# Optimization experiments

Measured on AMD Instinct MI355X. Metric: run time of the kernel, lower is better.

The kernel has to match this reference:

```python
import jax, jax.numpy as jnp
import numpy as np

EPS = 1e-5

def lrelu(x):
    return jnp.where(x >= 0, x, 0.1 * x)

def bn_eval(x, g, b, m, v):
    # eval-mode BatchNorm over the last (channel) axis
    return (x - m) * (g * jax.lax.rsqrt(v + EPS)) + b

def setup_inputs():
    key = jax.random.key(0)
    ks = jax.random.split(key, 12)
    Nq, K, Cin, Fc, Co = 20000, 32, 3, 64, 64
    q_points = jax.random.normal(ks[0], (Nq, Cin), jnp.float32)
    s_points = jax.random.normal(ks[1], (Nq, Cin), jnp.float32)
    feat = jax.random.normal(ks[2], (Nq, Fc), jnp.float32)
    # valid indices 0..Nq (Nq == shadow/pad row appended in forward)
    neighb_inds = jax.random.randint(ks[3], (Nq, K), 0, Nq + 1)
    def w(k, shape, fan_in):
        return jax.random.normal(k, shape, jnp.float32) / np.float32(np.sqrt(fan_in))
    W_pos2 = w(ks[4], (Fc, Cin), Cin)          # convpos2: Conv2d(Cin, Fc, 1)
    W_attn = w(ks[5], (Co * Cin, Fc), Fc)      # convattn: Conv2d(Fc, Co*Cin, 1)
    W_res = w(ks[6], (Co, Fc), Fc)             # residual 1x1 conv
    def bn(k, c):
        k1, k2, k3, k4 = jax.random.split(k, 4)
        return (jax.random.normal(k1, (c,), jnp.float32) * 0.1 + 1.0,
                jax.random.normal(k2, (c,), jnp.float32) * 0.1,
                jax.random.normal(k3, (c,), jnp.float32) * 0.1,
                jax.random.uniform(k4, (c,), jnp.float32) * 0.5 + 0.5)
    bq = bn(ks[7], Fc); bp = bn(ks[8], Cin); b1 = bn(ks[9], Co); br = bn(ks[10], Co)
    return dict(q_points=q_points, s_points=s_points, neighb_inds=neighb_inds, feat=feat,
                W_pos2=W_pos2, W_attn=W_attn, W_res=W_res,
                bnq_g=bq[0], bnq_b=bq[1], bnq_m=bq[2], bnq_v=bq[3],
                bnp_g=bp[0], bnp_b=bp[1], bnp_m=bp[2], bnp_v=bp[3],
                bn1_g=b1[0], bn1_b=b1[1], bn1_m=b1[2], bn1_v=b1[3],
                bnr_g=br[0], bnr_b=br[1], bnr_m=br[2], bnr_v=br[3])

def reference(q_points, s_points, neighb_inds, feat, W_pos2, W_attn, W_res,
              bnq_g, bnq_b, bnq_m, bnq_v, bnp_g, bnp_b, bnp_m, bnp_v,
              bn1_g, bn1_b, bn1_m, bn1_v, bnr_g, bnr_b, bnr_m, bnr_v):
    Nq, Cin = q_points.shape
    Fc = feat.shape[1]
    Co = W_res.shape[0]
    K = neighb_inds.shape[1]
    # append shadow (zero) row for out-of-range neighbor indices
    s_pad = jnp.concatenate([s_points, jnp.zeros((1, Cin), s_points.dtype)], 0)
    f_pad = jnp.concatenate([feat, jnp.zeros((1, Fc), feat.dtype)], 0)
    xg = s_pad[neighb_inds]                      # [Nq,K,Cin] EFR_P gather
    yg = f_pad[neighb_inds]                      # [Nq,K,Fc]  EFR_F gather
    x_v = xg - q_points[:, None, :]              # [Nq,K,Cin] values
    x_q = lrelu(bn_eval(feat, bnq_g, bnq_b, bnq_m, bnq_v))          # [Nq,Fc]
    pos0 = lrelu(bn_eval(s_points, bnp_g, bnp_b, bnp_m, bnp_v))     # [Nq,Cin]
    pos = (pos0[:, None, :] - x_v) @ W_pos2.T                       # [Nq,K,Fc]
    attn = x_q[:, None, :] - yg + pos                               # [Nq,K,Fc]
    attn = jax.nn.softmax(attn / jnp.sqrt(jnp.float32(Fc)), axis=1) # softmax over K
    attn = (attn @ W_attn.T).reshape(Nq, K, Co, Cin)                # [Nq,K,Co,Cin]
    y_e = jnp.einsum('nkoi,nki->nko', attn, x_v)                    # [Nq,K,Co]
    y_e = lrelu(bn_eval(y_e, bn1_g, bn1_b, bn1_m, bn1_v))
    res = bn_eval(yg @ W_res.T, bnr_g, bnr_b, bnr_m, bnr_v)         # [Nq,K,Co]
    y_e = lrelu(y_e + res)
    return y_e.max(axis=1)                                          # [Nq,Co]
```

## Files before the change

### kernel.cpp

```cpp
#include <hip/hip_runtime.h>
#include <math.h>

#define KNB 32
#define FC 64
#define CO 64
#define EPS 1e-5f
#define NBLOCKS 1024
#define CL 0.180336880095853f

typedef __attribute__((ext_vector_type(8))) short short8;
typedef __attribute__((ext_vector_type(4))) float floatx4;

#if __has_builtin(__builtin_amdgcn_exp2f)
#define EXP2F(x) __builtin_amdgcn_exp2f(x)
#else
#define EXP2F(x) exp2f(x)
#endif
#if __has_builtin(__builtin_amdgcn_rcpf)
#define RCPF(x) __builtin_amdgcn_rcpf(x)
#else
#define RCPF(x) (1.f / (x))
#endif

__device__ __forceinline__ unsigned int pkbf(float a, float b) {
    unsigned int ua = (__float_as_uint(a) + 0x8000u) >> 16;
    unsigned int ub = (__float_as_uint(b) + 0x8000u) & 0xFFFF0000u;
    return ua | ub;
}
__device__ __forceinline__ short f2bf(float x) {
    return (short)((__float_as_uint(x) + 0x8000u) >> 16);
}
__device__ __forceinline__ float lrelu(float x) { return fmaxf(x, 0.1f * x); }

__global__ __launch_bounds__(256, 4) void GCT_61272003445298_kernel(
    const float* __restrict__ q_points,
    const float* __restrict__ s_points,
    const int*   __restrict__ neighb,
    const float* __restrict__ feat,
    const float* __restrict__ W_pos2,
    const float* __restrict__ W_attn,
    const float* __restrict__ W_res,
    const float* __restrict__ bnq_g, const float* __restrict__ bnq_b,
    const float* __restrict__ bnq_m, const float* __restrict__ bnq_v,
    const float* __restrict__ bnp_g, const float* __restrict__ bnp_b,
    const float* __restrict__ bnp_m, const float* __restrict__ bnp_v,
    const float* __restrict__ bn1_g, const float* __restrict__ bn1_b,
    const float* __restrict__ bn1_m, const float* __restrict__ bn1_v,
    const float* __restrict__ bnr_g, const float* __restrict__ bnr_b,
    const float* __restrict__ bnr_m, const float* __restrict__ bnr_v,
    float* __restrict__ out, int Nq)
{
    const int t = threadIdx.x;
    const int wv = t >> 6;
    const int lane = t & 63;
    const int cc = lane & 15, quad = lane >> 4;
    const int o = wv * 16 + cc;

    const int qB  = t >> 7;
    const int kg  = lane >> 3;
    const int fqB = (((t >> 6) & 1) << 3) + (lane & 7);

    __shared__ __align__(16) short sA1[64 * 72];
    __shared__ __align__(16) short sA2[64 * 72];
    __shared__ float sXv[64][4];
    __shared__ __align__(16) float sWp2[192];
    __shared__ __align__(16) float sQs[64], sQb[64];

    if (t < 192) sWp2[t] = CL * W_pos2[t];
    if (t < 64) {
        float sc = bnq_g[t] * rsqrtf(bnq_v[t] + EPS);
        sQs[t] = sc; sQb[t] = bnq_b[t] - bnq_m[t] * sc;
    }
    float ps[3], pb[3];
    #pragma unroll
    for (int i = 0; i < 3; ++i) {
        float sc = bnp_g[i] * rsqrtf(bnp_v[i] + EPS);
        ps[i] = sc; pb[i] = bnp_b[i] - bnp_m[i] * sc;
    }
    const float e1s = bn1_g[o] * rsqrtf(bn1_v[o] + EPS);
    const float e1b = bn1_b[o] - bn1_m[o] * e1s;
    const float ers = bnr_g[o] * rsqrtf(bnr_v[o] + EPS);
    const float erb = bnr_b[o] - bnr_m[o] * ers;

    short8 bW[4][2];
    #pragma unroll
    for (int ty = 0; ty < 4; ++ty) {
        const float* wrow = (ty < 3) ? (W_attn + (long)(o * 3 + ty) * FC)
                                     : (W_res  + (long)o * FC);
        #pragma unroll
        for (int ks = 0; ks < 2; ++ks) {
            int k0 = ks * 32 + quad * 8;
            float4 w0 = *(const float4*)(wrow + k0);
            float4 w1 = *(const float4*)(wrow + k0 + 4);
            short8 b;
            b[0] = f2bf(w0.x); b[1] = f2bf(w0.y); b[2] = f2bf(w0.z); b[3] = f2bf(w0.w);
            b[4] = f2bf(w1.x); b[5] = f2bf(w1.y); b[6] = f2bf(w1.z); b[7] = f2bf(w1.w);
            bW[ty][ks] = b;
        }
    }
    __syncthreads();

    float wp[12];
    *(float4*)&wp[0] = *(const float4*)&sWp2[fqB * 12];
    *(float4*)&wp[4] = *(const float4*)&sWp2[fqB * 12 + 4];
    *(float4*)&wp[8] = *(const float4*)&sWp2[fqB * 12 + 8];

    const float4* __restrict__ feat4 = (const float4*)feat;
    const bool xvWriter = ((t & 0x47) == 0);

    const int npair = (Nq + 1) >> 1;
    for (int p = blockIdx.x; p < npair; p += NBLOCKS) {
        const long n0 = 2L * p;
        long n1 = n0 + 1;
        const bool has1 = (n1 < Nq);
        if (!has1) n1 = n0;
        const long nn = qB ? n1 : n0;

        float nqp0 = -q_points[nn * 3 + 0];
        float nqp1 = -q_points[nn * 3 + 1];
        float nqp2 = -q_points[nn * 3 + 2];
        float p0 = lrelu(fmaf(s_points[nn * 3 + 0], ps[0], pb[0]));
        float p1 = lrelu(fmaf(s_points[nn * 3 + 1], ps[1], pb[1]));
        float p2 = lrelu(fmaf(s_points[nn * 3 + 2], ps[2], pb[2]));
        int4 idx4 = *(const int4*)(neighb + nn * KNB + kg * 4);

        float4 qs4 = *(const float4*)&sQs[fqB * 4];
        float4 qb4 = *(const float4*)&sQb[fqB * 4];
        float4 fx  = feat4[(int)(nn * 16) + fqB];
        float4 xqc;
        {
            float x0 = lrelu(fmaf(fx.x, qs4.x, qb4.x));
            float x1 = lrelu(fmaf(fx.y, qs4.y, qb4.y));
            float x2 = lrelu(fmaf(fx.z, qs4.z, qb4.z));
            float x3 = lrelu(fmaf(fx.w, qs4.w, qb4.w));
            xqc.x = fmaf(p0, wp[0], fmaf(p1, wp[1],  fmaf(p2, wp[2],  CL * x0)));
            xqc.y = fmaf(p0, wp[3], fmaf(p1, wp[4],  fmaf(p2, wp[5],  CL * x1)));
            xqc.z = fmaf(p0, wp[6], fmaf(p1, wp[7],  fmaf(p2, wp[8],  CL * x2)));
            xqc.w = fmaf(p0, wp[9], fmaf(p1, wp[10], fmaf(p2, wp[11], CL * x3)));
        }

        float ev[4][4];
        float s0 = 0.f, s1 = 0.f, s2 = 0.f, s3 = 0.f;
        #pragma unroll
        for (int j = 0; j < 4; ++j) {
            const int idx = ((const int*)&idx4)[j];
            const int row = qB * 32 + kg * 4 + j;
            const float sel = (idx < Nq) ? 1.f : 0.f;
            const int idc = (idx < Nq) ? idx : 0;
            float4 y = feat4[idc * 16 + fqB];
            y.x *= sel; y.y *= sel; y.z *= sel; y.w *= sel;
            uint2 pk; pk.x = pkbf(y.x, y.y); pk.y = pkbf(y.z, y.w);
            *(uint2*)(sA2 + row * 72 + fqB * 4) = pk;
            float xv0 = fmaf(s_points[idc * 3 + 0], sel, nqp0);
            float xv1 = fmaf(s_points[idc * 3 + 1], sel, nqp1);
            float xv2 = fmaf(s_points[idc * 3 + 2], sel, nqp2);
            if (xvWriter) {
                sXv[row][0] = xv0; sXv[row][1] = xv1; sXv[row][2] = xv2;
                sXv[row][3] = 0.f;
            }
            float l0 = fmaf(y.x, -CL, xqc.x);
            l0 = fmaf(-xv0, wp[0], l0); l0 = fmaf(-xv1, wp[1], l0); l0 = fmaf(-xv2, wp[2], l0);
            float l1 = fmaf(y.y, -CL, xqc.y);
            l1 = fmaf(-xv0, wp[3], l1); l1 = fmaf(-xv1, wp[4], l1); l1 = fmaf(-xv2, wp[5], l1);
            float l2 = fmaf(y.z, -CL, xqc.z);
            l2 = fmaf(-xv0, wp[6], l2); l2 = fmaf(-xv1, wp[7], l2); l2 = fmaf(-xv2, wp[8], l2);
            float l3 = fmaf(y.w, -CL, xqc.w);
            l3 = fmaf(-xv0, wp[9], l3); l3 = fmaf(-xv1, wp[10], l3); l3 = fmaf(-xv2, wp[11], l3);
            ev[j][0] = EXP2F(l0); ev[j][1] = EXP2F(l1);
            ev[j][2] = EXP2F(l2); ev[j][3] = EXP2F(l3);
            s0 += ev[j][0]; s1 += ev[j][1]; s2 += ev[j][2]; s3 += ev[j][3];
        }
        s0 += __shfl_xor(s0, 8); s0 += __shfl_xor(s0, 16); s0 += __shfl_xor(s0, 32);
        s1 += __shfl_xor(s1, 8); s1 += __shfl_xor(s1, 16); s1 += __shfl_xor(s1, 32);
        s2 += __shfl_xor(s2, 8); s2 += __shfl_xor(s2, 16); s2 += __shfl_xor(s2, 32);
        s3 += __shfl_xor(s3, 8); s3 += __shfl_xor(s3, 16); s3 += __shfl_xor(s3, 32);
        const float i0 = RCPF(s0), i1 = RCPF(s1), i2 = RCPF(s2), i3 = RCPF(s3);
        #pragma unroll
        for (int j = 0; j < 4; ++j) {
            const int row = qB * 32 + kg * 4 + j;
            uint2 pw;
            pw.x = pkbf(ev[j][0] * i0, ev[j][1] * i1);
            pw.y = pkbf(ev[j][2] * i2, ev[j][3] * i3);
            *(uint2*)(sA1 + row * 72 + fqB * 4) = pw;
        }
        __syncthreads();

        float m0 = -1e30f, m1 = -1e30f;
        #pragma unroll
        for (int mt = 0; mt < 4; ++mt) {
            floatx4 acc[4];
            #pragma unroll
            for (int ty = 0; ty < 4; ++ty) acc[ty] = (floatx4){0.f, 0.f, 0.f, 0.f};
            int r0 = mt * 16 + cc;
            #pragma unroll
            for (int ks = 0; ks < 2; ++ks) {
                int kof = ks * 32 + quad * 8;
                short8 a1 = *(const short8*)(sA1 + r0 * 72 + kof);
                short8 a2 = *(const short8*)(sA2 + r0 * 72 + kof);
                acc[0] = __builtin_amdgcn_mfma_f32_16x16x32_bf16(a1, bW[0][ks], acc[0], 0, 0, 0);
                acc[1] = __builtin_amdgcn_mfma_f32_16x16x32_bf16(a1, bW[1][ks], acc[1], 0, 0, 0);
                acc[2] = __builtin_amdgcn_mfma_f32_16x16x32_bf16(a1, bW[2][ks], acc[2], 0, 0, 0);
                acc[3] = __builtin_amdgcn_mfma_f32_16x16x32_bf16(a2, bW[3][ks], acc[3], 0, 0, 0);
            }
            #pragma unroll
            for (int reg = 0; reg < 4; ++reg) {
                int r = mt * 16 + quad * 4 + reg;
                float4 xv = *(const float4*)&sXv[r][0];
                float y = acc[0][reg] * xv.x + acc[1][reg] * xv.y + acc[2][reg] * xv.z;
                float ybn = lrelu(y * e1s + e1b);
                float rbn = acc[3][reg] * ers + erb;
                float v = lrelu(ybn + rbn);
                if (mt < 2) m0 = fmaxf(m0, v); else m1 = fmaxf(m1, v);
            }
        }
        m0 = fmaxf(m0, __shfl_xor(m0, 16));
        m0 = fmaxf(m0, __shfl_xor(m0, 32));
        m1 = fmaxf(m1, __shfl_xor(m1, 16));
        m1 = fmaxf(m1, __shfl_xor(m1, 32));
        if (lane < 16) {
            out[n0 * CO + o] = m0;
            if (has1) out[n1 * CO + o] = m1;
        }
        __syncthreads();
    }
}

extern "C" void kernel_launch(void* const* d_in, const int* in_sizes, int n_in,
                              void* d_out, int out_size, void* d_ws, size_t ws_size,
                              hipStream_t stream) {
    const float* q_points = (const float*)d_in[0];
    const float* s_points = (const float*)d_in[1];
    const int*   neighb   = (const int*)  d_in[2];
    const float* feat     = (const float*)d_in[3];
    const float* W_pos2   = (const float*)d_in[4];
    const float* W_attn   = (const float*)d_in[5];
    const float* W_res    = (const float*)d_in[6];
    const float* bnq_g = (const float*)d_in[7];
    const float* bnq_b = (const float*)d_in[8];
    const float* bnq_m = (const float*)d_in[9];
    const float* bnq_v = (const float*)d_in[10];
    const float* bnp_g = (const float*)d_in[11];
    const float* bnp_b = (const float*)d_in[12];
    const float* bnp_m = (const float*)d_in[13];
    const float* bnp_v = (const float*)d_in[14];
    const float* bn1_g = (const float*)d_in[15];
    const float* bn1_b = (const float*)d_in[16];
    const float* bn1_m = (const float*)d_in[17];
    const float* bn1_v = (const float*)d_in[18];
    const float* bnr_g = (const float*)d_in[19];
    const float* bnr_b = (const float*)d_in[20];
    const float* bnr_m = (const float*)d_in[21];
    const float* bnr_v = (const float*)d_in[22];
    float* out = (float*)d_out;

    int Nq = in_sizes[0] / 3;

    hipLaunchKernelGGL(GCT_61272003445298_kernel,
                       dim3(NBLOCKS), dim3(256), 0, stream,
                       q_points, s_points, neighb, feat, W_pos2, W_attn, W_res,
                       bnq_g, bnq_b, bnq_m, bnq_v,
                       bnp_g, bnp_b, bnp_m, bnp_v,
                       bn1_g, bn1_b, bn1_m, bn1_v,
                       bnr_g, bnr_b, bnr_m, bnr_v,
                       out, Nq);
}
```

Before: 161.4 us.

## Fold BN scales into bf16 weights, pack float2 math, hoist final bias/lrelu past max

Folds the bn1 and residual BN scales into the bf16 MFMA weight operands. The final residual bias add and leaky ReLU move after the max over neighbours, which is valid because both are monotone, cutting per-element epilogue ALU work. The softmax logit arithmetic is rewritten with 2-wide float vectors so the compiler can emit packed FMA instructions, and bf16 packing uses the HIP intrinsic. The grid grows to 1280 blocks and launch bounds ask for 5 blocks per SM, which trades register budget for occupancy and may cause spills.

```diff
diff --git a/kernel.cpp b/kernel.cpp
--- a/kernel.cpp
+++ b/kernel.cpp
@@ -1,15 +1,17 @@
 #include <hip/hip_runtime.h>
+#include <hip/hip_bf16.h>
 #include <math.h>
 
 #define KNB 32
 #define FC 64
 #define CO 64
 #define EPS 1e-5f
-#define NBLOCKS 1024
+#define NBLOCKS 1280
 #define CL 0.180336880095853f
 
 typedef __attribute__((ext_vector_type(8))) short short8;
 typedef __attribute__((ext_vector_type(4))) float floatx4;
+typedef __attribute__((ext_vector_type(2))) float float2v;
 
 #if __has_builtin(__builtin_amdgcn_exp2f)
 #define EXP2F(x) __builtin_amdgcn_exp2f(x)
@@ -22,17 +24,20 @@
 #define RCPF(x) (1.f / (x))
 #endif
 
-__device__ __forceinline__ unsigned int pkbf(float a, float b) {
-    unsigned int ua = (__float_as_uint(a) + 0x8000u) >> 16;
-    unsigned int ub = (__float_as_uint(b) + 0x8000u) & 0xFFFF0000u;
-    return ua | ub;
-}
-__device__ __forceinline__ short f2bf(float x) {
-    return (short)((__float_as_uint(x) + 0x8000u) >> 16);
-}
+__device__ __forceinline__ unsigned pk2(float a, float b) {
+    __hip_bfloat162 h = __float22bfloat162_rn(float2{a, b});
+    unsigned u; __builtin_memcpy(&u, &h, 4); return u;
+}
+__device__ __forceinline__ unsigned pk2v(float2v v) { return pk2(v.x, v.y); }
 __device__ __forceinline__ float lrelu(float x) { return fmaxf(x, 0.1f * x); }
-
-__global__ __launch_bounds__(256, 4) void GCT_61272003445298_kernel(
+__device__ __forceinline__ float2v fma2(float2v a, float2v b, float2v c) {
+    return __builtin_elementwise_fma(a, b, c);
+}
+__device__ __forceinline__ float2v lrelu2(float2v x) {
+    return __builtin_elementwise_max(x, 0.1f * x);
+}
+
+__global__ __launch_bounds__(256, 5) void GCT_61272003445298_kernel(
     const float* __restrict__ q_points,
     const float* __restrict__ s_points,
     const int*   __restrict__ neighb,
@@ -55,7 +60,6 @@
     const int lane = t & 63;
     const int cc = lane & 15, quad = lane >> 4;
     const int o = wv * 16 + cc;
-
     const int qB  = t >> 7;
     const int kg  = lane >> 3;
     const int fqB = (((t >> 6) & 1) << 3) + (lane & 7);
@@ -71,12 +75,12 @@
         float sc = bnq_g[t] * rsqrtf(bnq_v[t] + EPS);
         sQs[t] = sc; sQb[t] = bnq_b[t] - bnq_m[t] * sc;
     }
-    float ps[3], pb[3];
-    #pragma unroll
-    for (int i = 0; i < 3; ++i) {
-        float sc = bnp_g[i] * rsqrtf(bnp_v[i] + EPS);
-        ps[i] = sc; pb[i] = bnp_b[i] - bnp_m[i] * sc;
-    }
+    const float ps0 = bnp_g[0] * rsqrtf(bnp_v[0] + EPS);
+    const float ps1 = bnp_g[1] * rsqrtf(bnp_v[1] + EPS);
+    const float ps2 = bnp_g[2] * rsqrtf(bnp_v[2] + EPS);
+    const float pb0 = bnp_b[0] - bnp_m[0] * ps0;
+    const float pb1 = bnp_b[1] - bnp_m[1] * ps1;
+    const float pb2 = bnp_b[2] - bnp_m[2] * ps2;
     const float e1s = bn1_g[o] * rsqrtf(bn1_v[o] + EPS);
     const float e1b = bn1_b[o] - bn1_m[o] * e1s;
     const float ers = bnr_g[o] * rsqrtf(bnr_v[o] + EPS);
@@ -87,26 +91,33 @@
     for (int ty = 0; ty < 4; ++ty) {
         const float* wrow = (ty < 3) ? (W_attn + (long)(o * 3 + ty) * FC)
                                      : (W_res  + (long)o * FC);
+        const float sc = (ty < 3) ? e1s : ers;
         #pragma unroll
         for (int ks = 0; ks < 2; ++ks) {
             int k0 = ks * 32 + quad * 8;
             float4 w0 = *(const float4*)(wrow + k0);
             float4 w1 = *(const float4*)(wrow + k0 + 4);
-            short8 b;
-            b[0] = f2bf(w0.x); b[1] = f2bf(w0.y); b[2] = f2bf(w0.z); b[3] = f2bf(w0.w);
-            b[4] = f2bf(w1.x); b[5] = f2bf(w1.y); b[6] = f2bf(w1.z); b[7] = f2bf(w1.w);
-            bW[ty][ks] = b;
+            uint4 pv;
+            pv.x = pk2(w0.x * sc, w0.y * sc);
+            pv.y = pk2(w0.z * sc, w0.w * sc);
+            pv.z = pk2(w1.x * sc, w1.y * sc);
+            pv.w = pk2(w1.z * sc, w1.w * sc);
+            __builtin_memcpy(&bW[ty][ks], &pv, 16);
         }
     }
     __syncthreads();
 
-    float wp[12];
-    *(float4*)&wp[0] = *(const float4*)&sWp2[fqB * 12];
-    *(float4*)&wp[4] = *(const float4*)&sWp2[fqB * 12 + 4];
-    *(float4*)&wp[8] = *(const float4*)&sWp2[fqB * 12 + 8];
-
+    float2v wpa[3], wpb[3];
+    {
+        const float* w = &sWp2[fqB * 12];
+        wpa[0] = (float2v){w[0], w[3]};  wpa[1] = (float2v){w[1], w[4]};
+        wpa[2] = (float2v){w[2], w[5]};
+        wpb[0] = (float2v){w[6], w[9]};  wpb[1] = (float2v){w[7], w[10]};
+        wpb[2] = (float2v){w[8], w[11]};
+    }
+    const float4 qs4 = *(const float4*)&sQs[fqB * 4];
+    const float4 qb4 = *(const float4*)&sQb[fqB * 4];
     const float4* __restrict__ feat4 = (const float4*)feat;
-    const bool xvWriter = ((t & 0x47) == 0);
 
     const int npair = (Nq + 1) >> 1;
     for (int p = blockIdx.x; p < npair; p += NBLOCKS) {
@@ -116,85 +127,88 @@
         if (!has1) n1 = n0;
         const long nn = qB ? n1 : n0;
 
-        float nqp0 = -q_points[nn * 3 + 0];
-        float nqp1 = -q_points[nn * 3 + 1];
-        float nqp2 = -q_points[nn * 3 + 2];
-        float p0 = lrelu(fmaf(s_points[nn * 3 + 0], ps[0], pb[0]));
-        float p1 = lrelu(fmaf(s_points[nn * 3 + 1], ps[1], pb[1]));
-        float p2 = lrelu(fmaf(s_points[nn * 3 + 2], ps[2], pb[2]));
-        int4 idx4 = *(const int4*)(neighb + nn * KNB + kg * 4);
-
-        float4 qs4 = *(const float4*)&sQs[fqB * 4];
-        float4 qb4 = *(const float4*)&sQb[fqB * 4];
-        float4 fx  = feat4[(int)(nn * 16) + fqB];
-        float4 xqc;
+        const float nq0 = -q_points[nn * 3 + 0];
+        const float nq1 = -q_points[nn * 3 + 1];
+        const float nq2 = -q_points[nn * 3 + 2];
+        const float pp0 = lrelu(fmaf(s_points[nn * 3 + 0], ps0, pb0));
+        const float pp1 = lrelu(fmaf(s_points[nn * 3 + 1], ps1, pb1));
+        const float pp2 = lrelu(fmaf(s_points[nn * 3 + 2], ps2, pb2));
+        const int4 idx4 = *(const int4*)(neighb + nn * KNB + kg * 4);
+
+        float2v xqcA, xqcB;
         {
-            float x0 = lrelu(fmaf(fx.x, qs4.x, qb4.x));
-            float x1 = lrelu(fmaf(fx.y, qs4.y, qb4.y));
-            float x2 = lrelu(fmaf(fx.z, qs4.z, qb4.z));
-            float x3 = lrelu(fmaf(fx.w, qs4.w, qb4.w));
-            xqc.x = fmaf(p0, wp[0], fmaf(p1, wp[1],  fmaf(p2, wp[2],  CL * x0)));
-            xqc.y = fmaf(p0, wp[3], fmaf(p1, wp[4],  fmaf(p2, wp[5],  CL * x1)));
-            xqc.z = fmaf(p0, wp[6], fmaf(p1, wp[7],  fmaf(p2, wp[8],  CL * x2)));
-            xqc.w = fmaf(p0, wp[9], fmaf(p1, wp[10], fmaf(p2, wp[11], CL * x3)));
-        }
-
-        float ev[4][4];
-        float s0 = 0.f, s1 = 0.f, s2 = 0.f, s3 = 0.f;
+            const float4 fx = feat4[(int)(nn * 16) + fqB];
+            float2v xqA = lrelu2(fma2((float2v){fx.x, fx.y},
+                                      (float2v){qs4.x, qs4.y},
+                                      (float2v){qb4.x, qb4.y}));
+            float2v xqB = lrelu2(fma2((float2v){fx.z, fx.w},
+                                      (float2v){qs4.z, qs4.w},
+                                      (float2v){qb4.z, qb4.w}));
+            const float2v v0 = (float2v){pp0, pp0};
+            const float2v v1 = (float2v){pp1, pp1};
+            const float2v v2 = (float2v){pp2, pp2};
+            xqcA = fma2(v0, wpa[0], fma2(v1, wpa[1], fma2(v2, wpa[2], CL * xqA)));
+            xqcB = fma2(v0, wpb[0], fma2(v1, wpb[1], fma2(v2, wpb[2], CL * xqB)));
+        }
+
+        short* a1b = &sA1[(qB * 32 + kg * 4) * 72 + fqB * 4];
+        short* a2b = &sA2[(qB * 32 + kg * 4) * 72 + fqB * 4];
+        float2v evA[4], evB[4];
+        float2v sumA = (float2v){0.f, 0.f}, sumB = (float2v){0.f, 0.f};
         #pragma unroll
         for (int j = 0; j < 4; ++j) {
             const int idx = ((const int*)&idx4)[j];
-            const int row = qB * 32 + kg * 4 + j;
             const float sel = (idx < Nq) ? 1.f : 0.f;
             const int idc = (idx < Nq) ? idx : 0;
             float4 y = feat4[idc * 16 + fqB];
             y.x *= sel; y.y *= sel; y.z *= sel; y.w *= sel;
-            uint2 pk; pk.x = pkbf(y.x, y.y); pk.y = pkbf(y.z, y.w);
-            *(uint2*)(sA2 + row * 72 + fqB * 4) = pk;
-            float xv0 = fmaf(s_points[idc * 3 + 0], sel, nqp0);
-            float xv1 = fmaf(s_points[idc * 3 + 1], sel, nqp1);
-            float xv2 = fmaf(s_points[idc * 3 + 2], sel, nqp2);
-            if (xvWriter) {
-                sXv[row][0] = xv0; sXv[row][1] = xv1; sXv[row][2] = xv2;
-                sXv[row][3] = 0.f;
+            uint2 pk; pk.x = pk2(y.x, y.y); pk.y = pk2(y.z, y.w);
+            *(uint2*)(a2b + j * 72) = pk;
+            const float xv0 = fmaf(s_points[idc * 3 + 0], sel, nq0);
+            const float xv1 = fmaf(s_points[idc * 3 + 1], sel, nq1);
+            const float xv2 = fmaf(s_points[idc * 3 + 2], sel, nq2);
+            if (fqB == 0) {
+                float4 xvv = {xv0, xv1, xv2, 0.f};
+                *(float4*)&sXv[qB * 32 + kg * 4 + j][0] = xvv;
             }
-            float l0 = fmaf(y.x, -CL, xqc.x);
-            l0 = fmaf(-xv0, wp[0], l0); l0 = fmaf(-xv1, wp[1], l0); l0 = fmaf(-xv2, wp[2], l0);
-            float l1 = fmaf(y.y, -CL, xqc.y);
-            l1 = fmaf(-xv0, wp[3], l1); l1 = fmaf(-xv1, wp[4], l1); l1 = fmaf(-xv2, wp[5], l1);
-            float l2 = fmaf(y.z, -CL, xqc.z);
-            l2 = fmaf(-xv0, wp[6], l2); l2 = fmaf(-xv1, wp[7], l2); l2 = fmaf(-xv2, wp[8], l2);
-            float l3 = fmaf(y.w, -CL, xqc.w);
-            l3 = fmaf(-xv0, wp[9], l3); l3 = fmaf(-xv1, wp[10], l3); l3 = fmaf(-xv2, wp[11], l3);
-            ev[j][0] = EXP2F(l0); ev[j][1] = EXP2F(l1);
-            ev[j][2] = EXP2F(l2); ev[j][3] = EXP2F(l3);
-            s0 += ev[j][0]; s1 += ev[j][1]; s2 += ev[j][2]; s3 += ev[j][3];
-        }
+            const float2v m0 = (float2v){-xv0, -xv0};
+            const float2v m1 = (float2v){-xv1, -xv1};
+            const float2v m2 = (float2v){-xv2, -xv2};
+            float2v lA = fma2((float2v){y.x, y.y}, (float2v){-CL, -CL}, xqcA);
+            lA = fma2(m0, wpa[0], lA); lA = fma2(m1, wpa[1], lA); lA = fma2(m2, wpa[2], lA);
+            float2v lB = fma2((float2v){y.z, y.w}, (float2v){-CL, -CL}, xqcB);
+            lB = fma2(m0, wpb[0], lB); lB = fma2(m1, wpb[1], lB); lB = fma2(m2, wpb[2], lB);
+            evA[j] = (float2v){EXP2F(lA.x), EXP2F(lA.y)};
+            evB[j] = (float2v){EXP2F(lB.x), EXP2F(lB.y)};
+            sumA = sumA + evA[j];
+            sumB = sumB + evB[j];
+        }
+        float s0 = sumA.x, s1 = sumA.y, s2 = sumB.x, s3 = sumB.y;
         s0 += __shfl_xor(s0, 8); s0 += __shfl_xor(s0, 16); s0 += __shfl_xor(s0, 32);
         s1 += __shfl_xor(s1, 8); s1 += __shfl_xor(s1, 16); s1 += __shfl_xor(s1, 32);
         s2 += __shfl_xor(s2, 8); s2 += __shfl_xor(s2, 16); s2 += __shfl_xor(s2, 32);
         s3 += __shfl_xor(s3, 8); s3 += __shfl_xor(s3, 16); s3 += __shfl_xor(s3, 32);
-        const float i0 = RCPF(s0), i1 = RCPF(s1), i2 = RCPF(s2), i3 = RCPF(s3);
+        const float2v invA = (float2v){RCPF(s0), RCPF(s1)};
+        const float2v invB = (float2v){RCPF(s2), RCPF(s3)};
         #pragma unroll
         for (int j = 0; j < 4; ++j) {
-            const int row = qB * 32 + kg * 4 + j;
             uint2 pw;
-            pw.x = pkbf(ev[j][0] * i0, ev[j][1] * i1);
-            pw.y = pkbf(ev[j][2] * i2, ev[j][3] * i3);
-            *(uint2*)(sA1 + row * 72 + fqB * 4) = pw;
+            pw.x = pk2v(evA[j] * invA);
+            pw.y = pk2v(evB[j] * invB);
+            *(uint2*)(a1b + j * 72) = pw;
         }
         __syncthreads();
 
-        float m0 = -1e30f, m1 = -1e30f;
+        float m0r = -1e30f, m1r = -1e30f;
         #pragma unroll
         for (int mt = 0; mt < 4; ++mt) {
             floatx4 acc[4];
             #pragma unroll
             for (int ty = 0; ty < 4; ++ty) acc[ty] = (floatx4){0.f, 0.f, 0.f, 0.f};
-            int r0 = mt * 16 + cc;
+            const int r0 = mt * 16 + cc;
             #pragma unroll
             for (int ks = 0; ks < 2; ++ks) {
-                int kof = ks * 32 + quad * 8;
+                const int kof = ks * 32 + quad * 8;
                 short8 a1 = *(const short8*)(sA1 + r0 * 72 + kof);
                 short8 a2 = *(const short8*)(sA2 + r0 * 72 + kof);
                 acc[0] = __builtin_amdgcn_mfma_f32_16x16x32_bf16(a1, bW[0][ks], acc[0], 0, 0, 0);
@@ -204,22 +218,20 @@
             }
             #pragma unroll
             for (int reg = 0; reg < 4; ++reg) {
-                int r = mt * 16 + quad * 4 + reg;
+                const int r = mt * 16 + quad * 4 + reg;
                 float4 xv = *(const float4*)&sXv[r][0];
                 float y = acc[0][reg] * xv.x + acc[1][reg] * xv.y + acc[2][reg] * xv.z;
-                float ybn = lrelu(y * e1s + e1b);
-                float rbn = acc[3][reg] * ers + erb;
-                float v = lrelu(ybn + rbn);
-                if (mt < 2) m0 = fmaxf(m0, v); else m1 = fmaxf(m1, v);
+                float v = lrelu(y + e1b) + acc[3][reg];
+                if (mt < 2) m0r = fmaxf(m0r, v); else m1r = fmaxf(m1r, v);
             }
         }
-        m0 = fmaxf(m0, __shfl_xor(m0, 16));
-        m0 = fmaxf(m0, __shfl_xor(m0, 32));
-        m1 = fmaxf(m1, __shfl_xor(m1, 16));
-        m1 = fmaxf(m1, __shfl_xor(m1, 32));
+        m0r = fmaxf(m0r, __shfl_xor(m0r, 16));
+        m0r = fmaxf(m0r, __shfl_xor(m0r, 32));
+        m1r = fmaxf(m1r, __shfl_xor(m1r, 16));
+        m1r = fmaxf(m1r, __shfl_xor(m1r, 32));
         if (lane < 16) {
-            out[n0 * CO + o] = m0;
-            if (has1) out[n1 * CO + o] = m1;
+            out[n0 * CO + o] = lrelu(m0r + erb);
+            if (has1) out[n1 * CO + o] = lrelu(m1r + erb);
         }
         __syncthreads();
     }
```

Measured after the change: 197.0 us. 22.1% more time.
